# Kernel optimization log

Measured on AMD Instinct MI355X. Metric: run time of the kernel, lower is better.

The kernel has to match this reference:

```python
import jax, jax.numpy as jnp
import numpy as np

B, D, U = 64, 256, 256

def setup_inputs() -> dict:
    key = jax.random.key(0)
    ks = jax.random.split(key, 16)
    init_mu = 0.05
    inputs = jax.random.normal(ks[0], (B, D), jnp.float32)
    prev_state = 0.1 * jax.random.normal(ks[1], (B, U), jnp.float32)
    A = jax.random.normal(ks[2], (B, U, U), jnp.float32)
    # symmetric, diagonally boosted covariance-like state
    Sigma_state = 0.01 * (A + jnp.swapaxes(A, 1, 2)) + 0.1 * jnp.eye(U, dtype=jnp.float32)
    def w(k, shape):
        return init_mu * jax.random.normal(k, shape, jnp.float32)
    def s(k):
        return jax.random.uniform(k, (U,), jnp.float32, -4.5, -2.2)
    return {
        'inputs': inputs, 'prev_state': prev_state, 'Sigma_state': Sigma_state,
        'U_z': w(ks[3], (D, U)), 'uz_sigma': s(ks[4]), 'W_z': w(ks[5], (U, U)), 'wz_sigma': s(ks[6]),
        'U_r': w(ks[7], (D, U)), 'ur_sigma': s(ks[8]), 'W_r': w(ks[9], (U, U)), 'wr_sigma': s(ks[10]),
        'U_h': w(ks[11], (D, U)), 'uh_sigma': s(ks[12]), 'W_h': w(ks[13], (U, U)), 'wh_sigma': s(ks[14]),
    }

def _outer(a, b):  # [B,u],[B,u] -> [B,u,u]
    return a[:, :, None] * b[:, None, :]

def _quad(W, S):  # W^T @ S @ W, S is [B,u,u]
    return jnp.matmul(jnp.matmul(W.T, S), W)

def _x_sigma_w(x, sv):  # ||x||^2 * diag(softplus sigma)
    return jnp.sum(x * x, axis=1)[:, None, None] * jnp.diag(sv)

def _tr_sigma_w(S, sv):  # trace(S) * diag(softplus sigma)
    return jnp.trace(S, axis1=1, axis2=2)[:, None, None] * jnp.diag(sv)

def _hadamard_sigma(S1, S2, m1, m2):
    # S1*S2 + diag(m1) S2 diag(m1) + diag(m2) S1 diag(m2) as elementwise/broadcast
    return S1 * S2 + _outer(m1, m1) * S2 + _outer(m2, m2) * S1

def reference(inputs, prev_state, Sigma_state, U_z, uz_sigma, W_z, wz_sigma,
              U_r, ur_sigma, W_r, wr_sigma, U_h, uh_sigma, W_h, wh_sigma):
    sp = jax.nn.softplus
    # --- z gate ---
    az = inputs @ U_z + prev_state @ W_z
    z = jax.nn.sigmoid(az)
    gz = z * (1.0 - z)  # d sigmoid
    Sz = (_quad(W_z, Sigma_state) + _x_sigma_w(prev_state, sp(wz_sigma))
          + _tr_sigma_w(Sigma_state, sp(wz_sigma)) + _x_sigma_w(inputs, sp(uz_sigma)))
    Sigma_out_z = Sz * _outer(gz, gz)
    # --- r gate ---
    ar = inputs @ U_r + prev_state @ W_r
    r = jax.nn.sigmoid(ar)
    gr = r * (1.0 - r)
    Sr = (_quad(W_r, Sigma_state) + _x_sigma_w(prev_state, sp(wr_sigma))
          + _tr_sigma_w(Sigma_state, sp(wr_sigma)) + _x_sigma_w(inputs, sp(ur_sigma)))
    Sigma_out_r = Sr * _outer(gr, gr)
    # --- h candidate ---
    g_in = prev_state * r
    ah = inputs @ U_h + g_in @ W_h
    h = jnp.tanh(ah)
    gh = 1.0 - h * h  # d tanh
    sigma_g = _hadamard_sigma(Sigma_state, Sigma_out_r, prev_state, r)
    Sh = (_quad(W_h, sigma_g) + _x_sigma_w(g_in, sp(wh_sigma))
          + _tr_sigma_w(sigma_g, sp(wh_sigma)) + _x_sigma_w(inputs, sp(uh_sigma)))
    Sigma_out_h = Sh * _outer(gh, gh)
    # --- output combination ---
    mu_out = z * prev_state + (1.0 - z) * h
    sigma_a = _hadamard_sigma(Sigma_out_z, Sigma_state, z, prev_state)
    sigma_b = _hadamard_sigma(Sigma_out_z, Sigma_out_h, 1.0 - z, h)
    Sigma_out = (sigma_a + sigma_b
                 - Sigma_out_z * _outer(prev_state, h)
                 - Sigma_out_z * _outer(h, prev_state))
    Sigma_out = jnp.where(jnp.isnan(Sigma_out) | jnp.isinf(Sigma_out),
                          jnp.zeros_like(Sigma_out), Sigma_out)
    eye = jnp.eye(Sigma_out.shape[-1], dtype=Sigma_out.dtype)
    d = jnp.abs(jnp.diagonal(Sigma_out, axis1=1, axis2=2))
    Sigma_out = Sigma_out * (1.0 - eye) + d[:, :, None] * eye
    return mu_out, Sigma_out
```

## Files before the change

### kernel.cpp

```cpp
#include <hip/hip_runtime.h>
#include <math.h>

#define UDIM 256
#define BATCH 64
#define MATN 65536
#define PITCH 280

typedef __bf16 bf16x8 __attribute__((ext_vector_type(8)));
typedef float  f32x4  __attribute__((ext_vector_type(4)));

__device__ __forceinline__ float softplusf(float x) { return log1pf(expf(x)); }
__device__ __forceinline__ float sigmoidf_(float x) { return 1.f/(1.f+expf(-x)); }

__device__ __forceinline__ bf16x8 frag_load(const __bf16* base, int rt, int kt, int lane) {
  return *(const bf16x8*)(base + (((size_t)(rt*8 + kt))*64 + lane)*8);
}

__device__ __forceinline__ bf16x8 cvt8(const float* p) {
  const float4 f0 = *(const float4*)p;
  const float4 f1 = *(const float4*)(p + 4);
  bf16x8 v;
  v[0]=(__bf16)f0.x; v[1]=(__bf16)f0.y; v[2]=(__bf16)f0.z; v[3]=(__bf16)f0.w;
  v[4]=(__bf16)f1.x; v[5]=(__bf16)f1.y; v[6]=(__bf16)f1.z; v[7]=(__bf16)f1.w;
  return v;
}

__global__ __launch_bounds__(256) void prep_w(
    const float* __restrict__ Uz, const float* __restrict__ Wz,
    const float* __restrict__ Ur, const float* __restrict__ Wr,
    const float* __restrict__ Uh, const float* __restrict__ Wh,
    __bf16* __restrict__ Fu_z, __bf16* __restrict__ Fw_z,
    __bf16* __restrict__ Fu_r, __bf16* __restrict__ Fw_r,
    __bf16* __restrict__ Fu_h, __bf16* __restrict__ Fw_h,
    const float* __restrict__ S, const float* __restrict__ x,
    const float* __restrict__ prev, float* __restrict__ scal,
    __bf16* __restrict__ Sf)
{
  const int u = blockIdx.x;
  const int t = threadIdx.x;
  if (u >= 112) {
    const int c = u - 112;
    const int bx = c & 3, by = (c >> 2) & 3, b = c >> 4;
    const size_t sb = (size_t)b * MATN;
#pragma unroll
    for (int ss = 0; ss < 2; ++ss) {
      const int s = t + ss*256;
      const int chunk = s >> 6, lane = s & 63;
      const int rt_l = chunk >> 1, kt_l = chunk & 1;
      const int row = by*64 + rt_l*16 + (lane & 15);
      const int col = bx*64 + kt_l*32 + (lane >> 4)*8;
      const bf16x8 v = cvt8(S + sb + (size_t)row*UDIM + col);
      *(bf16x8*)(Sf + sb + (((size_t)((by*4 + rt_l)*8 + bx*2 + kt_l))*64 + lane)*8) = v;
    }
    return;
  }
  if (u >= 96) {
    const int blk = u - 96;
    const int b = blk*4 + (t >> 6), l = t & 63;
    const float4 xv = *(const float4*)(x + b*UDIM + l*4);
    float s0 = xv.x*xv.x + xv.y*xv.y + xv.z*xv.z + xv.w*xv.w;
    const float4 pv = *(const float4*)(prev + b*UDIM + l*4);
    float s1 = pv.x*pv.x + pv.y*pv.y + pv.z*pv.z + pv.w*pv.w;
    float s2 = 0.f;
#pragma unroll
    for (int e = 0; e < 4; ++e)
      s2 += S[(size_t)b*MATN + (size_t)(l*4 + e)*257];
    for (int off = 32; off; off >>= 1) {
      s0 += __shfl_down(s0, off);
      s1 += __shfl_down(s1, off);
      s2 += __shfl_down(s2, off);
    }
    if (l == 0) {
      atomicAdd(&scal[b], s0);
      atomicAdd(&scal[64 + b], s1);
      atomicAdd(&scal[128 + b], s2);
    }
    return;
  }
  const int mat = u >> 4, tl = u & 15;
  const int n0 = (tl & 3)*64, k0 = (tl >> 2)*64;
  const float* W; __bf16* F;
  switch (mat) {
    case 0: W = Uz; F = Fu_z; break;  case 1: W = Wz; F = Fw_z; break;
    case 2: W = Ur; F = Fu_r; break;  case 3: W = Wr; F = Fw_r; break;
    case 4: W = Uh; F = Fu_h; break;  default: W = Wh; F = Fw_h; break;
  }
  __shared__ float tile[64][65];
  const int tx = t & 15, ty = t >> 4;
#pragma unroll
  for (int rr = 0; rr < 4; ++rr) {
    const int row = ty*4 + rr;
    const float4 f = *(const float4*)(W + (size_t)(k0 + row)*UDIM + n0 + tx*4);
    tile[row][tx*4+0] = f.x; tile[row][tx*4+1] = f.y;
    tile[row][tx*4+2] = f.z; tile[row][tx*4+3] = f.w;
  }
  __syncthreads();
#pragma unroll
  for (int ss = 0; ss < 2; ++ss) {
    const int s = t + ss*256;
    const int rt_l = s >> 7, kt_l = (s >> 6) & 1, lane = s & 63;
    const int nl = rt_l*16 + (lane & 15), kb = kt_l*32 + (lane >> 4)*8;
    __align__(16) __bf16 tmp[8];
#pragma unroll
    for (int e = 0; e < 8; ++e) tmp[e] = (__bf16)tile[kb + e][nl];
    *(uint4*)(F + (((size_t)((((n0 >> 4) + rt_l)*8) + (k0 >> 5) + kt_l))*64 + lane)*8)
        = *(const uint4*)tmp;
  }
}

__global__ __launch_bounds__(256) void gates_zr(
    const float* __restrict__ x, const float* __restrict__ prev,
    const __bf16* __restrict__ Fu_z, const __bf16* __restrict__ Fw_z,
    const __bf16* __restrict__ Fu_r, const __bf16* __restrict__ Fw_r,
    float* __restrict__ zb, float* __restrict__ rb,
    float* __restrict__ gzb, float* __restrict__ grb,
    float* __restrict__ gin, float* __restrict__ scal)
{
  const int bid = blockIdx.x;
  const int gate = bid >> 4, jt = (bid >> 2) & 3, ni = bid & 3;
  const int t = threadIdx.x, w = t >> 6, l = t & 63, r = l & 15, q = l >> 4;
  const __bf16* FU = gate ? Fu_r : Fu_z;
  const __bf16* FW = gate ? Fw_r : Fw_z;
  const int mrow = w*16 + r;
  f32x4 acc = {};
#pragma unroll
  for (int ks = 0; ks < 16; ++ks) {
    const int k0 = ks*32;
    const float* asrc; const __bf16* B; int kk;
    if (k0 < 256) { asrc = x    + (size_t)mrow*UDIM + k0         + q*8; B = FU; kk = k0; }
    else          { asrc = prev + (size_t)mrow*UDIM + (k0 - 256) + q*8; B = FW; kk = k0 - 256; }
    const bf16x8 af = cvt8(asrc);
    const bf16x8 bv = frag_load(B, jt*4 + ni, kk >> 5, l);
    acc = __builtin_amdgcn_mfma_f32_16x16x32_bf16(af, bv, acc, 0, 0, 0);
  }
  const int n = jt*64 + ni*16 + r;
  if (gate == 0) {
#pragma unroll
    for (int v = 0; v < 4; ++v) {
      const int m = w*16 + q*4 + v;
      const float zv = sigmoidf_(acc[v]);
      zb[m*UDIM + n]  = zv;
      gzb[m*UDIM + n] = zv * (1.f - zv);
    }
  } else {
    float ggp[4];
#pragma unroll
    for (int v = 0; v < 4; ++v) {
      const int m = w*16 + q*4 + v;
      const float rv = sigmoidf_(acc[v]);
      const float pv = prev[m*UDIM + n];
      const float g2 = pv * rv;
      rb[m*UDIM + n]  = rv;
      grb[m*UDIM + n] = rv * (1.f - rv);
      gin[m*UDIM + n] = g2;
      ggp[v] = g2 * g2;
    }
#pragma unroll
    for (int s = 1; s < 16; s <<= 1)
#pragma unroll
      for (int v = 0; v < 4; ++v) ggp[v] += __shfl_xor(ggp[v], s);
    if (r == 0)
#pragma unroll
      for (int v = 0; v < 4; ++v)
        atomicAdd(&scal[192 + w*16 + q*4 + v], ggp[v]);
  }
}

__global__ __launch_bounds__(256, 2) void quad_zr_gh(
    const float* __restrict__ S, const __bf16* __restrict__ Sf,
    const float* __restrict__ prev,
    const float* __restrict__ rb, const float* __restrict__ gzb,
    const float* __restrict__ grb,
    const float* __restrict__ wz_s, const float* __restrict__ uz_s,
    const float* __restrict__ wr_s, const float* __restrict__ ur_s,
    const __bf16* __restrict__ Fw_z, const __bf16* __restrict__ Fw_r,
    float* __restrict__ scal, __bf16* __restrict__ Szb, __bf16* __restrict__ G,
    const float* __restrict__ x, const float* __restrict__ gin,
    const float* __restrict__ zb,
    const __bf16* __restrict__ Fu_h, const __bf16* __restrict__ Fw_h,
    float* __restrict__ hb, float* __restrict__ ghb, float* __restrict__ mu_out)
{
  const int bid = blockIdx.x;
  const int t = threadIdx.x, w = t >> 6, l = t & 63, r = l & 15, q = l >> 4;

  if (bid < 4) {
    const int jt = bid;
    const int mrow = w*16 + r;
    f32x4 acc[4] = {};
#pragma unroll
    for (int ks = 0; ks < 16; ++ks) {
      const int k0 = ks*32;
      const float* asrc; const __bf16* B; int kk;
      if (k0 < 256) { asrc = x   + (size_t)mrow*UDIM + k0         + q*8; B = Fu_h; kk = k0; }
      else          { asrc = gin + (size_t)mrow*UDIM + (k0 - 256) + q*8; B = Fw_h; kk = k0 - 256; }
      const bf16x8 af = cvt8(asrc);
#pragma unroll
      for (int ni = 0; ni < 4; ++ni) {
        const bf16x8 bv = frag_load(B, jt*4 + ni, kk >> 5, l);
        acc[ni] = __builtin_amdgcn_mfma_f32_16x16x32_bf16(af, bv, acc[ni], 0, 0, 0);
      }
    }
#pragma unroll
    for (int ni = 0; ni < 4; ++ni) {
      const int n = jt*64 + ni*16 + r;
#pragma unroll
      for (int v = 0; v < 4; ++v) {
        const int m = w*16 + q*4 + v;
        const float hv = tanhf(acc[ni][v]);
        const float zv = zb[m*UDIM + n];
        hb[m*UDIM + n]  = hv;
        ghb[m*UDIM + n] = 1.f - hv*hv;
        mu_out[m*UDIM + n] = zv * prev[m*UDIM + n] + (1.f - zv) * hv;
      }
    }
    return;
  }

  const int id = bid - 4;
  const int gater = (id < 256);
  const int rem = id & 255;
  const int sg = rem >> 6, b = rem & 63;
  const size_t sb = (size_t)b * MATN;
  const __bf16* Sfb = Sf + sb;
  const __bf16* FW = gater ? Fw_r : Fw_z;

  __shared__ __align__(16) __bf16 T[4*16*PITCH];

  f32x4 a[4][4] = {};
#pragma unroll
  for (int kt = 0; kt < 8; ++kt) {
    bf16x8 af[4];
#pragma unroll
    for (int sl = 0; sl < 4; ++sl) af[sl] = frag_load(FW, sg*4 + sl, kt, l);
#pragma unroll
    for (int ct = 0; ct < 4; ++ct) {
      const bf16x8 bv = frag_load(Sfb, w*4 + ct, kt, l);
#pragma unroll
      for (int sl = 0; sl < 4; ++sl)
        a[sl][ct] = __builtin_amdgcn_mfma_f32_16x16x32_bf16(af[sl], bv, a[sl][ct], 0, 0, 0);
    }
  }
#pragma unroll
  for (int sl = 0; sl < 4; ++sl)
#pragma unroll
    for (int ct = 0; ct < 4; ++ct)
#pragma unroll
      for (int v = 0; v < 4; ++v)
        T[sl*16*PITCH + (q*4 + v)*PITCH + w*64 + ct*16 + r] = (__bf16)a[sl][ct][v];
  __syncthreads();

  f32x4 qx[4][4] = {};
#pragma unroll
  for (int kt = 0; kt < 8; ++kt) {
    bf16x8 bw[4];
#pragma unroll
    for (int ct = 0; ct < 4; ++ct) bw[ct] = frag_load(FW, w*4 + ct, kt, l);
#pragma unroll
    for (int sl = 0; sl < 4; ++sl) {
      const bf16x8 at = *(const bf16x8*)&T[sl*16*PITCH + r*PITCH + kt*32 + q*8];
#pragma unroll
      for (int ct = 0; ct < 4; ++ct)
        qx[sl][ct] = __builtin_amdgcn_mfma_f32_16x16x32_bf16(at, bw[ct], qx[sl][ct], 0, 0, 0);
    }
  }

  const float xx = scal[b];
  const float dscal = scal[64 + b] + scal[128 + b];

  if (!gater) {
#pragma unroll
    for (int sl = 0; sl < 4; ++sl) {
      const int s4 = sg*4 + sl;
      const int ib = s4*16 + q*4;
      const f32x4 g4 = *(const f32x4*)(gzb + b*UDIM + ib);
      __align__(16) __bf16 o16[16];
#pragma unroll
      for (int ct = 0; ct < 4; ++ct) {
        const int j = (w*4 + ct)*16 + r;
        const float gj = gzb[b*UDIM + j];
#pragma unroll
        for (int v = 0; v < 4; ++v) {
          const int i = ib + v;
          float qv = qx[sl][ct][v];
          if (i == j) qv += dscal*softplusf(wz_s[i]) + xx*softplusf(uz_s[i]);
          o16[ct*4 + v] = (__bf16)(qv * g4[v] * gj);
        }
      }
      __bf16* dst = Szb + ((size_t)(b*16 + s4)*256 + t)*16;
      *(uint4*)dst       = *(const uint4*)&o16[0];
      *(uint4*)(dst + 8) = *(const uint4*)&o16[8];
    }
  } else {
    __syncthreads();
    float trg = 0.f;
#pragma unroll
    for (int sl = 0; sl < 4; ++sl) {
      const int s4 = sg*4 + sl;
      const int ib = s4*16 + q*4;
      const f32x4 g4 = *(const f32x4*)(grb + b*UDIM + ib);
      const f32x4 p4 = *(const f32x4*)(prev + b*UDIM + ib);
      const f32x4 r4 = *(const f32x4*)(rb + b*UDIM + ib);
#pragma unroll
      for (int ct = 0; ct < 4; ++ct) {
        const int j = (w*4 + ct)*16 + r;
        const float gj = grb[b*UDIM + j];
        const float pj = prev[b*UDIM + j];
        const float rj = rb[b*UDIM + j];
#pragma unroll
        for (int v = 0; v < 4; ++v) {
          const int i = ib + v;
          float qv = qx[sl][ct][v];
          if (i == j) qv += dscal*softplusf(wr_s[i]) + xx*softplusf(ur_s[i]);
          const float Sg = qv * g4[v] * gj;
          const float sv = S[sb + (size_t)i*UDIM + j];
          const float go = Sg*(sv + p4[v]*pj) + r4[v]*rj*sv;
          T[sl*16*PITCH + (q*4 + v)*PITCH + w*64 + ct*16 + r] = (__bf16)go;
          if (i == j) trg += go;
        }
      }
    }
    if (trg != 0.f) atomicAdd(&scal[256 + b], trg);
    __syncthreads();
#pragma unroll
    for (int sl = 0; sl < 4; ++sl)
#pragma unroll
      for (int ee = 0; ee < 2; ++ee) {
        const int e = t + ee*256;
        const int kt = e >> 6, le = e & 63;
        const uint4 vv = *(const uint4*)&T[sl*16*PITCH + (le & 15)*PITCH + kt*32 + (le >> 4)*8];
        *(uint4*)(G + sb + (((size_t)((sg*4 + sl)*8 + kt))*64 + le)*8) = vv;
      }
  }
}

__global__ __launch_bounds__(256, 2) void quad_h(
    const float* __restrict__ S, const __bf16* __restrict__ Szb,
    const float* __restrict__ prev, const float* __restrict__ zb,
    const float* __restrict__ hb, const float* __restrict__ ghb,
    const float* __restrict__ wh_s, const float* __restrict__ uh_s,
    const __bf16* __restrict__ Fw_h, const __bf16* __restrict__ G,
    const float* __restrict__ scal, float* __restrict__ out_sig)
{
  const int bid = blockIdx.x;
  const int sg = bid >> 6, b = bid & 63;
  const size_t sb = (size_t)b * MATN;
  const int t = threadIdx.x, w = t >> 6, l = t & 63, r = l & 15, q = l >> 4;
  const __bf16* Gb = G + sb;

  __shared__ __align__(16) __bf16 Th[2*16*PITCH];

  f32x4 ah[2][4] = {};
#pragma unroll
  for (int kt = 0; kt < 8; ++kt) {
    bf16x8 af[2];
#pragma unroll
    for (int sl = 0; sl < 2; ++sl) af[sl] = frag_load(Fw_h, sg*2 + sl, kt, l);
#pragma unroll
    for (int ct = 0; ct < 4; ++ct) {
      const bf16x8 bv = frag_load(Gb, w*4 + ct, kt, l);
#pragma unroll
      for (int sl = 0; sl < 2; ++sl)
        ah[sl][ct] = __builtin_amdgcn_mfma_f32_16x16x32_bf16(af[sl], bv, ah[sl][ct], 0, 0, 0);
    }
  }
#pragma unroll
  for (int sl = 0; sl < 2; ++sl)
#pragma unroll
    for (int ct = 0; ct < 4; ++ct)
#pragma unroll
      for (int v = 0; v < 4; ++v)
        Th[sl*16*PITCH + (q*4 + v)*PITCH + w*64 + ct*16 + r] = (__bf16)ah[sl][ct][v];
  __syncthreads();

  f32x4 qh[2][4] = {};
#pragma unroll
  for (int kt = 0; kt < 8; ++kt) {
    bf16x8 bw[4];
#pragma unroll
    for (int ct = 0; ct < 4; ++ct) bw[ct] = frag_load(Fw_h, w*4 + ct, kt, l);
#pragma unroll
    for (int sl = 0; sl < 2; ++sl) {
      const bf16x8 at = *(const bf16x8*)&Th[sl*16*PITCH + r*PITCH + kt*32 + q*8];
#pragma unroll
      for (int ct = 0; ct < 4; ++ct)
        qh[sl][ct] = __builtin_amdgcn_mfma_f32_16x16x32_bf16(at, bw[ct], qh[sl][ct], 0, 0, 0);
    }
  }

  const float xx = scal[b];
  const float dscal = scal[192 + b] + scal[256 + b];

#pragma unroll
  for (int sl = 0; sl < 2; ++sl) {
    const int s4 = sg*2 + sl;
    const int ib = s4*16 + q*4;

    const __bf16* szp = Szb + ((size_t)(b*16 + s4)*256 + t)*16;
    __align__(16) __bf16 sz16[16];
    *(uint4*)&sz16[0] = *(const uint4*)szp;
    *(uint4*)&sz16[8] = *(const uint4*)(szp + 8);

    const f32x4 g4 = *(const f32x4*)(ghb + b*UDIM + ib);
    const f32x4 p4 = *(const f32x4*)(prev + b*UDIM + ib);
    const f32x4 z4 = *(const f32x4*)(zb + b*UDIM + ib);
    const f32x4 h4 = *(const f32x4*)(hb + b*UDIM + ib);

#pragma unroll
    for (int ct = 0; ct < 4; ++ct) {
      const int j = (w*4 + ct)*16 + r;
      const float gj = ghb[b*UDIM + j];
      const float pj = prev[b*UDIM + j];
      const float zj = zb[b*UDIM + j];
      const float hj = hb[b*UDIM + j];
#pragma unroll
      for (int v = 0; v < 4; ++v) {
        const int i = ib + v;
        float qv = qh[sl][ct][v];
        if (i == j) qv += dscal*softplusf(wh_s[i]) + xx*softplusf(uh_s[i]);
        const float Sg = qv * g4[v] * gj;
        const float sv = S[sb + (size_t)i*UDIM + j];
        const float sz = (float)sz16[ct*4 + v];
        float val = sv*(sz + z4[v]*zj)
                  + sz*(p4[v] - h4[v])*(pj - hj)
                  + Sg*(sz + (1.f - z4[v])*(1.f - zj));
        if (!isfinite(val)) val = 0.f;
        if (i == j) val = fabsf(val);
        out_sig[sb + (size_t)i*UDIM + j] = val;
      }
    }
  }
}

extern "C" void kernel_launch(void* const* d_in, const int* in_sizes, int n_in,
                              void* d_out, int out_size, void* d_ws, size_t ws_size,
                              hipStream_t stream) {
  const float* x    = (const float*)d_in[0];
  const float* prev = (const float*)d_in[1];
  const float* S    = (const float*)d_in[2];
  const float* Uz   = (const float*)d_in[3];
  const float* uz_s = (const float*)d_in[4];
  const float* Wz   = (const float*)d_in[5];
  const float* wz_s = (const float*)d_in[6];
  const float* Ur   = (const float*)d_in[7];
  const float* ur_s = (const float*)d_in[8];
  const float* Wr   = (const float*)d_in[9];
  const float* wr_s = (const float*)d_in[10];
  const float* Uh   = (const float*)d_in[11];
  const float* uh_s = (const float*)d_in[12];
  const float* Wh   = (const float*)d_in[13];
  const float* wh_s = (const float*)d_in[14];

  float* out_mu  = (float*)d_out;
  float* out_sig = out_mu + BATCH*UDIM;

  float* ws   = (float*)d_ws;
  float* zb   = ws;
  float* rb   = zb  + BATCH*UDIM;
  float* gzb  = rb  + BATCH*UDIM;
  float* grb  = gzb + BATCH*UDIM;
  float* gin  = grb + BATCH*UDIM;
  float* hb   = gin + BATCH*UDIM;
  float* ghb  = hb  + BATCH*UDIM;
  float* scal = ghb + BATCH*UDIM;
  __bf16* bws  = (__bf16*)(scal + 512);
  __bf16* Fu_z = bws;
  __bf16* Fw_z = Fu_z + MATN;
  __bf16* Fu_r = Fw_z + MATN;
  __bf16* Fw_r = Fu_r + MATN;
  __bf16* Fu_h = Fw_r + MATN;
  __bf16* Fw_h = Fu_h + MATN;
  const size_t BIG = (size_t)BATCH * MATN;
  __bf16* Szb = Fw_h + MATN;
  __bf16* G   = Szb + BIG;
  __bf16* Sf  = G + BIG;

  hipMemsetAsync(scal, 0, 512*sizeof(float), stream);

  prep_w<<<dim3(1136), 256, 0, stream>>>(Uz, Wz, Ur, Wr, Uh, Wh,
      Fu_z, Fw_z, Fu_r, Fw_r, Fu_h, Fw_h, S, x, prev, scal, Sf);
  gates_zr<<<dim3(32), 256, 0, stream>>>(x, prev,
      Fu_z, Fw_z, Fu_r, Fw_r, zb, rb, gzb, grb, gin, scal);
  quad_zr_gh<<<dim3(516), 256, 0, stream>>>(S, Sf, prev, rb, gzb, grb,
      wz_s, uz_s, wr_s, ur_s, Fw_z, Fw_r, scal, Szb, G,
      x, gin, zb, Fu_h, Fw_h, hb, ghb, out_mu);
  quad_h<<<dim3(512), 256, 0, stream>>>(S, Szb, prev, zb, hb, ghb,
      wh_s, uh_s, Fw_h, G, scal, out_sig);
}
```

Measured before the change: 172.0 us.

## Fuse four kernels into one persistent kernel with software grid barriers

Replaces the prep, gate, quad_zr and quad_h launches with a single 512-block kernel that separates the phases with a hierarchical atomic grid barrier. It also swaps the atomicAdd reductions for per-slot partial writes that are summed later, so the scalar buffer no longer needs a memset. The aim is to remove launch gaps and the tail idle time between dependent stages. In exchange, all 512 blocks must be co-resident (two per CU) or the barrier will deadlock, and spin-waiting adds its own overhead.

```diff
diff --git a/kernel.cpp b/kernel.cpp
--- a/kernel.cpp
+++ b/kernel.cpp
@@ -5,6 +5,9 @@
 #define BATCH 64
 #define MATN 65536
 #define PITCH 280
+#define NBLK 512
+#define GG_BASE 256
+#define TRG_BASE 1280
 
 typedef __bf16 bf16x8 __attribute__((ext_vector_type(8)));
 typedef float  f32x4  __attribute__((ext_vector_type(4)));
@@ -25,407 +28,411 @@
   return v;
 }
 
-__global__ __launch_bounds__(256) void prep_w(
-    const float* __restrict__ Uz, const float* __restrict__ Wz,
-    const float* __restrict__ Ur, const float* __restrict__ Wr,
-    const float* __restrict__ Uh, const float* __restrict__ Wh,
+__device__ __forceinline__ void gridbar(unsigned int* cnt, int bid, int t) {
+  __syncthreads();
+  if (t == 0) {
+    __threadfence();
+    unsigned int* lc = cnt + (bid & 7);
+    unsigned int* gc = cnt + 15;
+    if (atomicAdd(lc, 1u) == (unsigned)(NBLK/8 - 1)) atomicAdd(gc, 1u);
+    while (__hip_atomic_load(gc, __ATOMIC_RELAXED, __HIP_MEMORY_SCOPE_AGENT) < 8u)
+      __builtin_amdgcn_s_sleep(2);
+    __threadfence();
+  }
+  __syncthreads();
+}
+
+__global__ __launch_bounds__(256, 2) void fused(
+    const float* __restrict__ x, const float* __restrict__ prev,
+    const float* __restrict__ S,
+    const float* __restrict__ Uz, const float* __restrict__ uz_s,
+    const float* __restrict__ Wz, const float* __restrict__ wz_s,
+    const float* __restrict__ Ur, const float* __restrict__ ur_s,
+    const float* __restrict__ Wr, const float* __restrict__ wr_s,
+    const float* __restrict__ Uh, const float* __restrict__ uh_s,
+    const float* __restrict__ Wh, const float* __restrict__ wh_s,
+    float* __restrict__ out_mu, float* __restrict__ out_sig,
+    float* __restrict__ zb, float* __restrict__ rb,
+    float* __restrict__ gzb, float* __restrict__ grb,
+    float* __restrict__ gin, float* __restrict__ hb, float* __restrict__ ghb,
+    float* __restrict__ scal, unsigned int* __restrict__ bar,
     __bf16* __restrict__ Fu_z, __bf16* __restrict__ Fw_z,
     __bf16* __restrict__ Fu_r, __bf16* __restrict__ Fw_r,
     __bf16* __restrict__ Fu_h, __bf16* __restrict__ Fw_h,
-    const float* __restrict__ S, const float* __restrict__ x,
-    const float* __restrict__ prev, float* __restrict__ scal,
-    __bf16* __restrict__ Sf)
+    __bf16* __restrict__ Szb, __bf16* __restrict__ G, __bf16* __restrict__ Sf)
 {
-  const int u = blockIdx.x;
+  const int bid = blockIdx.x;
   const int t = threadIdx.x;
-  if (u >= 112) {
-    const int c = u - 112;
-    const int bx = c & 3, by = (c >> 2) & 3, b = c >> 4;
-    const size_t sb = (size_t)b * MATN;
+  const int w = t >> 6, l = t & 63, r = l & 15, q = l >> 4;
+
+  __shared__ __align__(16) unsigned char LDSU[4*16*PITCH*2];
+
+  if (bid < 96) {
+    const int mat = bid >> 4, tl = bid & 15;
+    const int n0 = (tl & 3)*64, k0 = (tl >> 2)*64;
+    const float* W; __bf16* F;
+    switch (mat) {
+      case 0: W = Uz; F = Fu_z; break;  case 1: W = Wz; F = Fw_z; break;
+      case 2: W = Ur; F = Fu_r; break;  case 3: W = Wr; F = Fw_r; break;
+      case 4: W = Uh; F = Fu_h; break;  default: W = Wh; F = Fw_h; break;
+    }
+    float (*tile)[65] = (float (*)[65])LDSU;
+    const int tx = t & 15, ty = t >> 4;
+#pragma unroll
+    for (int rr = 0; rr < 4; ++rr) {
+      const int row = ty*4 + rr;
+      const float4 f = *(const float4*)(W + (size_t)(k0 + row)*UDIM + n0 + tx*4);
+      tile[row][tx*4+0] = f.x; tile[row][tx*4+1] = f.y;
+      tile[row][tx*4+2] = f.z; tile[row][tx*4+3] = f.w;
+    }
+    __syncthreads();
 #pragma unroll
     for (int ss = 0; ss < 2; ++ss) {
       const int s = t + ss*256;
-      const int chunk = s >> 6, lane = s & 63;
-      const int rt_l = chunk >> 1, kt_l = chunk & 1;
-      const int row = by*64 + rt_l*16 + (lane & 15);
-      const int col = bx*64 + kt_l*32 + (lane >> 4)*8;
-      const bf16x8 v = cvt8(S + sb + (size_t)row*UDIM + col);
-      *(bf16x8*)(Sf + sb + (((size_t)((by*4 + rt_l)*8 + bx*2 + kt_l))*64 + lane)*8) = v;
-    }
-    return;
-  }
-  if (u >= 96) {
-    const int blk = u - 96;
-    const int b = blk*4 + (t >> 6), l = t & 63;
-    const float4 xv = *(const float4*)(x + b*UDIM + l*4);
+      const int rt_l = s >> 7, kt_l = (s >> 6) & 1, lane = s & 63;
+      const int nl = rt_l*16 + (lane & 15), kb = kt_l*32 + (lane >> 4)*8;
+      __align__(16) __bf16 tmp[8];
+#pragma unroll
+      for (int e = 0; e < 8; ++e) tmp[e] = (__bf16)tile[kb + e][nl];
+      *(uint4*)(F + (((size_t)((((n0 >> 4) + rt_l)*8) + (k0 >> 5) + kt_l))*64 + lane)*8)
+          = *(const uint4*)tmp;
+    }
+    __syncthreads();
+  } else if (bid < 112) {
+    const int blk = bid - 96;
+    const int b0 = blk*4 + (t >> 6);
+    const float4 xv = *(const float4*)(x + b0*UDIM + l*4);
     float s0 = xv.x*xv.x + xv.y*xv.y + xv.z*xv.z + xv.w*xv.w;
-    const float4 pv = *(const float4*)(prev + b*UDIM + l*4);
+    const float4 pv = *(const float4*)(prev + b0*UDIM + l*4);
     float s1 = pv.x*pv.x + pv.y*pv.y + pv.z*pv.z + pv.w*pv.w;
     float s2 = 0.f;
 #pragma unroll
     for (int e = 0; e < 4; ++e)
-      s2 += S[(size_t)b*MATN + (size_t)(l*4 + e)*257];
+      s2 += S[(size_t)b0*MATN + (size_t)(l*4 + e)*257];
     for (int off = 32; off; off >>= 1) {
       s0 += __shfl_down(s0, off);
       s1 += __shfl_down(s1, off);
       s2 += __shfl_down(s2, off);
     }
-    if (l == 0) {
-      atomicAdd(&scal[b], s0);
-      atomicAdd(&scal[64 + b], s1);
-      atomicAdd(&scal[128 + b], s2);
-    }
-    return;
-  }
-  const int mat = u >> 4, tl = u & 15;
-  const int n0 = (tl & 3)*64, k0 = (tl >> 2)*64;
-  const float* W; __bf16* F;
-  switch (mat) {
-    case 0: W = Uz; F = Fu_z; break;  case 1: W = Wz; F = Fw_z; break;
-    case 2: W = Ur; F = Fu_r; break;  case 3: W = Wr; F = Fw_r; break;
-    case 4: W = Uh; F = Fu_h; break;  default: W = Wh; F = Fw_h; break;
-  }
-  __shared__ float tile[64][65];
-  const int tx = t & 15, ty = t >> 4;
-#pragma unroll
-  for (int rr = 0; rr < 4; ++rr) {
-    const int row = ty*4 + rr;
-    const float4 f = *(const float4*)(W + (size_t)(k0 + row)*UDIM + n0 + tx*4);
-    tile[row][tx*4+0] = f.x; tile[row][tx*4+1] = f.y;
-    tile[row][tx*4+2] = f.z; tile[row][tx*4+3] = f.w;
-  }
-  __syncthreads();
-#pragma unroll
-  for (int ss = 0; ss < 2; ++ss) {
-    const int s = t + ss*256;
-    const int rt_l = s >> 7, kt_l = (s >> 6) & 1, lane = s & 63;
-    const int nl = rt_l*16 + (lane & 15), kb = kt_l*32 + (lane >> 4)*8;
-    __align__(16) __bf16 tmp[8];
-#pragma unroll
-    for (int e = 0; e < 8; ++e) tmp[e] = (__bf16)tile[kb + e][nl];
-    *(uint4*)(F + (((size_t)((((n0 >> 4) + rt_l)*8) + (k0 >> 5) + kt_l))*64 + lane)*8)
-        = *(const uint4*)tmp;
-  }
-}
-
-__global__ __launch_bounds__(256) void gates_zr(
-    const float* __restrict__ x, const float* __restrict__ prev,
-    const __bf16* __restrict__ Fu_z, const __bf16* __restrict__ Fw_z,
-    const __bf16* __restrict__ Fu_r, const __bf16* __restrict__ Fw_r,
-    float* __restrict__ zb, float* __restrict__ rb,
-    float* __restrict__ gzb, float* __restrict__ grb,
-    float* __restrict__ gin, float* __restrict__ scal)
-{
-  const int bid = blockIdx.x;
-  const int gate = bid >> 4, jt = (bid >> 2) & 3, ni = bid & 3;
-  const int t = threadIdx.x, w = t >> 6, l = t & 63, r = l & 15, q = l >> 4;
-  const __bf16* FU = gate ? Fu_r : Fu_z;
+    if (l == 0) { scal[b0] = s0; scal[64 + b0] = s1; scal[128 + b0] = s2; }
+  }
+  {
+    const int bb = bid & 63, hi = bid >> 6;
+    const size_t csb = (size_t)bb * MATN;
+#pragma unroll
+    for (int e2 = 0; e2 < 2; ++e2) {
+      const int c = (bb << 4) | (hi << 1) | e2;
+      const int bx = c & 3, by = (c >> 2) & 3;
+#pragma unroll
+      for (int ss = 0; ss < 2; ++ss) {
+        const int s = t + ss*256;
+        const int chunk = s >> 6, lane = s & 63;
+        const int rt_l = chunk >> 1, kt_l = chunk & 1;
+        const int row = by*64 + rt_l*16 + (lane & 15);
+        const int col = bx*64 + kt_l*32 + (lane >> 4)*8;
+        const bf16x8 v = cvt8(S + csb + (size_t)row*UDIM + col);
+        *(bf16x8*)(Sf + csb + (((size_t)((by*4 + rt_l)*8 + bx*2 + kt_l))*64 + lane)*8) = v;
+      }
+    }
+  }
+  gridbar(bar, bid, t);
+
+  const int gate = bid >> 8;
+  const int rem8 = bid & 255;
+  const int sg = rem8 >> 6, b = rem8 & 63;
+  const size_t sb = (size_t)b * MATN;
   const __bf16* FW = gate ? Fw_r : Fw_z;
-  const int mrow = w*16 + r;
-  f32x4 acc = {};
-#pragma unroll
-  for (int ks = 0; ks < 16; ++ks) {
-    const int k0 = ks*32;
-    const float* asrc; const __bf16* B; int kk;
-    if (k0 < 256) { asrc = x    + (size_t)mrow*UDIM + k0         + q*8; B = FU; kk = k0; }
-    else          { asrc = prev + (size_t)mrow*UDIM + (k0 - 256) + q*8; B = FW; kk = k0 - 256; }
-    const bf16x8 af = cvt8(asrc);
-    const bf16x8 bv = frag_load(B, jt*4 + ni, kk >> 5, l);
-    acc = __builtin_amdgcn_mfma_f32_16x16x32_bf16(af, bv, acc, 0, 0, 0);
-  }
-  const int n = jt*64 + ni*16 + r;
-  if (gate == 0) {
-#pragma unroll
-    for (int v = 0; v < 4; ++v) {
-      const int m = w*16 + q*4 + v;
-      const float zv = sigmoidf_(acc[v]);
-      zb[m*UDIM + n]  = zv;
-      gzb[m*UDIM + n] = zv * (1.f - zv);
-    }
-  } else {
-    float ggp[4];
-#pragma unroll
-    for (int v = 0; v < 4; ++v) {
-      const int m = w*16 + q*4 + v;
-      const float rv = sigmoidf_(acc[v]);
-      const float pv = prev[m*UDIM + n];
-      const float g2 = pv * rv;
-      rb[m*UDIM + n]  = rv;
-      grb[m*UDIM + n] = rv * (1.f - rv);
-      gin[m*UDIM + n] = g2;
-      ggp[v] = g2 * g2;
-    }
-#pragma unroll
-    for (int s = 1; s < 16; s <<= 1)
-#pragma unroll
-      for (int v = 0; v < 4; ++v) ggp[v] += __shfl_xor(ggp[v], s);
-    if (r == 0)
-#pragma unroll
-      for (int v = 0; v < 4; ++v)
-        atomicAdd(&scal[192 + w*16 + q*4 + v], ggp[v]);
-  }
-}
-
-__global__ __launch_bounds__(256, 2) void quad_zr_gh(
-    const float* __restrict__ S, const __bf16* __restrict__ Sf,
-    const float* __restrict__ prev,
-    const float* __restrict__ rb, const float* __restrict__ gzb,
-    const float* __restrict__ grb,
-    const float* __restrict__ wz_s, const float* __restrict__ uz_s,
-    const float* __restrict__ wr_s, const float* __restrict__ ur_s,
-    const __bf16* __restrict__ Fw_z, const __bf16* __restrict__ Fw_r,
-    float* __restrict__ scal, __bf16* __restrict__ Szb, __bf16* __restrict__ G,
-    const float* __restrict__ x, const float* __restrict__ gin,
-    const float* __restrict__ zb,
-    const __bf16* __restrict__ Fu_h, const __bf16* __restrict__ Fw_h,
-    float* __restrict__ hb, float* __restrict__ ghb, float* __restrict__ mu_out)
-{
-  const int bid = blockIdx.x;
-  const int t = threadIdx.x, w = t >> 6, l = t & 63, r = l & 15, q = l >> 4;
-
-  if (bid < 4) {
-    const int jt = bid;
+  __bf16* T = (__bf16*)LDSU;
+
+  if (bid < 32) {
+    const int gg_ = bid >> 4, jt_ = (bid >> 2) & 3, ni_ = bid & 3;
+    const __bf16* FU_ = gg_ ? Fu_r : Fu_z;
+    const __bf16* FW_ = gg_ ? Fw_r : Fw_z;
     const int mrow = w*16 + r;
-    f32x4 acc[4] = {};
+    f32x4 acc = {};
 #pragma unroll
     for (int ks = 0; ks < 16; ++ks) {
       const int k0 = ks*32;
-      const float* asrc; const __bf16* B; int kk;
-      if (k0 < 256) { asrc = x   + (size_t)mrow*UDIM + k0         + q*8; B = Fu_h; kk = k0; }
-      else          { asrc = gin + (size_t)mrow*UDIM + (k0 - 256) + q*8; B = Fw_h; kk = k0 - 256; }
+      const float* asrc; const __bf16* Bm; int kk;
+      if (k0 < 256) { asrc = x    + (size_t)mrow*UDIM + k0         + q*8; Bm = FU_; kk = k0; }
+      else          { asrc = prev + (size_t)mrow*UDIM + (k0 - 256) + q*8; Bm = FW_; kk = k0 - 256; }
       const bf16x8 af = cvt8(asrc);
-#pragma unroll
-      for (int ni = 0; ni < 4; ++ni) {
-        const bf16x8 bv = frag_load(B, jt*4 + ni, kk >> 5, l);
-        acc[ni] = __builtin_amdgcn_mfma_f32_16x16x32_bf16(af, bv, acc[ni], 0, 0, 0);
-      }
-    }
-#pragma unroll
-    for (int ni = 0; ni < 4; ++ni) {
-      const int n = jt*64 + ni*16 + r;
+      const bf16x8 bv = frag_load(Bm, jt_*4 + ni_, kk >> 5, l);
+      acc = __builtin_amdgcn_mfma_f32_16x16x32_bf16(af, bv, acc, 0, 0, 0);
+    }
+    const int n = jt_*64 + ni_*16 + r;
+    if (gg_ == 0) {
 #pragma unroll
       for (int v = 0; v < 4; ++v) {
         const int m = w*16 + q*4 + v;
-        const float hv = tanhf(acc[ni][v]);
+        const float zv = sigmoidf_(acc[v]);
+        zb[m*UDIM + n]  = zv;
+        gzb[m*UDIM + n] = zv * (1.f - zv);
+      }
+    } else {
+      float ggp[4];
+#pragma unroll
+      for (int v = 0; v < 4; ++v) {
+        const int m = w*16 + q*4 + v;
+        const float rv = sigmoidf_(acc[v]);
+        const float pv = prev[m*UDIM + n];
+        const float g2 = pv * rv;
+        rb[m*UDIM + n]  = rv;
+        grb[m*UDIM + n] = rv * (1.f - rv);
+        gin[m*UDIM + n] = g2;
+        ggp[v] = g2 * g2;
+      }
+#pragma unroll
+      for (int s2 = 1; s2 < 16; s2 <<= 1)
+#pragma unroll
+        for (int v = 0; v < 4; ++v) ggp[v] += __shfl_xor(ggp[v], s2);
+      if (r == 0)
+#pragma unroll
+        for (int v = 0; v < 4; ++v)
+          scal[GG_BASE + (w*16 + q*4 + v)*16 + (jt_*4 + ni_)] = ggp[v];
+    }
+  }
+
+  {
+    const __bf16* Sfb = Sf + sb;
+    f32x4 a[4][4] = {};
+#pragma unroll
+    for (int kt = 0; kt < 8; ++kt) {
+      bf16x8 af4[4];
+#pragma unroll
+      for (int sl = 0; sl < 4; ++sl) af4[sl] = frag_load(FW, sg*4 + sl, kt, l);
+#pragma unroll
+      for (int ct = 0; ct < 4; ++ct) {
+        const bf16x8 bv = frag_load(Sfb, w*4 + ct, kt, l);
+#pragma unroll
+        for (int sl = 0; sl < 4; ++sl)
+          a[sl][ct] = __builtin_amdgcn_mfma_f32_16x16x32_bf16(af4[sl], bv, a[sl][ct], 0, 0, 0);
+      }
+    }
+#pragma unroll
+    for (int sl = 0; sl < 4; ++sl)
+#pragma unroll
+      for (int ct = 0; ct < 4; ++ct)
+#pragma unroll
+        for (int v = 0; v < 4; ++v)
+          T[sl*16*PITCH + (q*4 + v)*PITCH + w*64 + ct*16 + r] = (__bf16)a[sl][ct][v];
+  }
+  gridbar(bar + 16, bid, t);
+
+  if (bid >= 32 && bid < 36) {
+    const int jt_h = bid - 32;
+    const int mrow = w*16 + r;
+    f32x4 acch[4] = {};
+#pragma unroll
+    for (int ks = 0; ks < 16; ++ks) {
+      const int k0 = ks*32;
+      const float* asrc; const __bf16* Bm; int kk;
+      if (k0 < 256) { asrc = x   + (size_t)mrow*UDIM + k0         + q*8; Bm = Fu_h; kk = k0; }
+      else          { asrc = gin + (size_t)mrow*UDIM + (k0 - 256) + q*8; Bm = Fw_h; kk = k0 - 256; }
+      const bf16x8 af = cvt8(asrc);
+#pragma unroll
+      for (int ni = 0; ni < 4; ++ni) {
+        const bf16x8 bv = frag_load(Bm, jt_h*4 + ni, kk >> 5, l);
+        acch[ni] = __builtin_amdgcn_mfma_f32_16x16x32_bf16(af, bv, acch[ni], 0, 0, 0);
+      }
+    }
+#pragma unroll
+    for (int ni = 0; ni < 4; ++ni) {
+      const int n = jt_h*64 + ni*16 + r;
+#pragma unroll
+      for (int v = 0; v < 4; ++v) {
+        const int m = w*16 + q*4 + v;
+        const float hv = tanhf(acch[ni][v]);
         const float zv = zb[m*UDIM + n];
         hb[m*UDIM + n]  = hv;
         ghb[m*UDIM + n] = 1.f - hv*hv;
-        mu_out[m*UDIM + n] = zv * prev[m*UDIM + n] + (1.f - zv) * hv;
-      }
-    }
-    return;
-  }
-
-  const int id = bid - 4;
-  const int gater = (id < 256);
-  const int rem = id & 255;
-  const int sg = rem >> 6, b = rem & 63;
-  const size_t sb = (size_t)b * MATN;
-  const __bf16* Sfb = Sf + sb;
-  const __bf16* FW = gater ? Fw_r : Fw_z;
-
-  __shared__ __align__(16) __bf16 T[4*16*PITCH];
-
-  f32x4 a[4][4] = {};
-#pragma unroll
-  for (int kt = 0; kt < 8; ++kt) {
-    bf16x8 af[4];
-#pragma unroll
-    for (int sl = 0; sl < 4; ++sl) af[sl] = frag_load(FW, sg*4 + sl, kt, l);
-#pragma unroll
-    for (int ct = 0; ct < 4; ++ct) {
-      const bf16x8 bv = frag_load(Sfb, w*4 + ct, kt, l);
+        out_mu[m*UDIM + n] = zv * prev[m*UDIM + n] + (1.f - zv) * hv;
+      }
+    }
+  }
+
+  {
+    f32x4 qx[4][4] = {};
+#pragma unroll
+    for (int kt = 0; kt < 8; ++kt) {
+      bf16x8 bw[4];
+#pragma unroll
+      for (int ct = 0; ct < 4; ++ct) bw[ct] = frag_load(FW, w*4 + ct, kt, l);
+#pragma unroll
+      for (int sl = 0; sl < 4; ++sl) {
+        const bf16x8 at = *(const bf16x8*)&T[sl*16*PITCH + r*PITCH + kt*32 + q*8];
+#pragma unroll
+        for (int ct = 0; ct < 4; ++ct)
+          qx[sl][ct] = __builtin_amdgcn_mfma_f32_16x16x32_bf16(at, bw[ct], qx[sl][ct], 0, 0, 0);
+      }
+    }
+
+    const float xx = scal[b];
+    const float dsc = scal[64 + b] + scal[128 + b];
+
+    if (gate == 0) {
+#pragma unroll
+      for (int sl = 0; sl < 4; ++sl) {
+        const int s4 = sg*4 + sl;
+        const int ib = s4*16 + q*4;
+        const f32x4 g4 = *(const f32x4*)(gzb + b*UDIM + ib);
+        __align__(16) __bf16 o16[16];
+#pragma unroll
+        for (int ct = 0; ct < 4; ++ct) {
+          const int j = (w*4 + ct)*16 + r;
+          const float gj = gzb[b*UDIM + j];
+#pragma unroll
+          for (int v = 0; v < 4; ++v) {
+            const int i = ib + v;
+            float qv = qx[sl][ct][v];
+            if (i == j) qv += dsc*softplusf(wz_s[i]) + xx*softplusf(uz_s[i]);
+            o16[ct*4 + v] = (__bf16)(qv * g4[v] * gj);
+          }
+        }
+        __bf16* dst = Szb + ((size_t)(b*16 + s4)*256 + t)*16;
+        *(uint4*)dst       = *(const uint4*)&o16[0];
+        *(uint4*)(dst + 8) = *(const uint4*)&o16[8];
+      }
+    } else {
+      __syncthreads();
+      float trgs[4] = {0.f, 0.f, 0.f, 0.f};
+#pragma unroll
+      for (int sl = 0; sl < 4; ++sl) {
+        const int s4 = sg*4 + sl;
+        const int ib = s4*16 + q*4;
+        const f32x4 g4 = *(const f32x4*)(grb + b*UDIM + ib);
+        const f32x4 p4 = *(const f32x4*)(prev + b*UDIM + ib);
+        const f32x4 r4 = *(const f32x4*)(rb + b*UDIM + ib);
+#pragma unroll
+        for (int ct = 0; ct < 4; ++ct) {
+          const int j = (w*4 + ct)*16 + r;
+          const float gj = grb[b*UDIM + j];
+          const float pj = prev[b*UDIM + j];
+          const float rj = rb[b*UDIM + j];
+#pragma unroll
+          for (int v = 0; v < 4; ++v) {
+            const int i = ib + v;
+            float qv = qx[sl][ct][v];
+            if (i == j) qv += dsc*softplusf(wr_s[i]) + xx*softplusf(ur_s[i]);
+            const float Sg = qv * g4[v] * gj;
+            const float sv = S[sb + (size_t)i*UDIM + j];
+            const float go = Sg*(sv + p4[v]*pj) + r4[v]*rj*sv;
+            T[sl*16*PITCH + (q*4 + v)*PITCH + w*64 + ct*16 + r] = (__bf16)go;
+            if (i == j) trgs[sl] += go;
+          }
+        }
+      }
+      if (w == sg) {
+#pragma unroll
+        for (int sl = 0; sl < 4; ++sl)
+#pragma unroll
+          for (int s2 = 1; s2 < 64; s2 <<= 1) trgs[sl] += __shfl_xor(trgs[sl], s2);
+        if (l == 0)
+#pragma unroll
+          for (int sl = 0; sl < 4; ++sl)
+            scal[TRG_BASE + b*16 + sg*4 + sl] = trgs[sl];
+      }
+      __syncthreads();
 #pragma unroll
       for (int sl = 0; sl < 4; ++sl)
-        a[sl][ct] = __builtin_amdgcn_mfma_f32_16x16x32_bf16(af[sl], bv, a[sl][ct], 0, 0, 0);
-    }
-  }
-#pragma unroll
-  for (int sl = 0; sl < 4; ++sl)
-#pragma unroll
-    for (int ct = 0; ct < 4; ++ct)
-#pragma unroll
-      for (int v = 0; v < 4; ++v)
-        T[sl*16*PITCH + (q*4 + v)*PITCH + w*64 + ct*16 + r] = (__bf16)a[sl][ct][v];
-  __syncthreads();
-
-  f32x4 qx[4][4] = {};
-#pragma unroll
-  for (int kt = 0; kt < 8; ++kt) {
-    bf16x8 bw[4];
-#pragma unroll
-    for (int ct = 0; ct < 4; ++ct) bw[ct] = frag_load(FW, w*4 + ct, kt, l);
-#pragma unroll
-    for (int sl = 0; sl < 4; ++sl) {
-      const bf16x8 at = *(const bf16x8*)&T[sl*16*PITCH + r*PITCH + kt*32 + q*8];
+#pragma unroll
+        for (int ee = 0; ee < 2; ++ee) {
+          const int e = t + ee*256;
+          const int kt = e >> 6, le = e & 63;
+          const uint4 vv = *(const uint4*)&T[sl*16*PITCH + (le & 15)*PITCH + kt*32 + (le >> 4)*8];
+          *(uint4*)(G + sb + (((size_t)((sg*4 + sl)*8 + kt))*64 + le)*8) = vv;
+        }
+    }
+  }
+  gridbar(bar + 32, bid, t);
+
+  {
+    const int b3 = bid & 63, sg2 = bid >> 6;
+    const size_t sb3 = (size_t)b3 * MATN;
+    const __bf16* Gb = G + sb3;
+    __bf16* Th = (__bf16*)LDSU;
+
+    f32x4 ah[2][4] = {};
+#pragma unroll
+    for (int kt = 0; kt < 8; ++kt) {
+      bf16x8 af2[2];
+#pragma unroll
+      for (int sl = 0; sl < 2; ++sl) af2[sl] = frag_load(Fw_h, sg2*2 + sl, kt, l);
+#pragma unroll
+      for (int ct = 0; ct < 4; ++ct) {
+        const bf16x8 bv = frag_load(Gb, w*4 + ct, kt, l);
+#pragma unroll
+        for (int sl = 0; sl < 2; ++sl)
+          ah[sl][ct] = __builtin_amdgcn_mfma_f32_16x16x32_bf16(af2[sl], bv, ah[sl][ct], 0, 0, 0);
+      }
+    }
+#pragma unroll
+    for (int sl = 0; sl < 2; ++sl)
 #pragma unroll
       for (int ct = 0; ct < 4; ++ct)
-        qx[sl][ct] = __builtin_amdgcn_mfma_f32_16x16x32_bf16(at, bw[ct], qx[sl][ct], 0, 0, 0);
-    }
-  }
-
-  const float xx = scal[b];
-  const float dscal = scal[64 + b] + scal[128 + b];
-
-  if (!gater) {
-#pragma unroll
-    for (int sl = 0; sl < 4; ++sl) {
-      const int s4 = sg*4 + sl;
+#pragma unroll
+        for (int v = 0; v < 4; ++v)
+          Th[sl*16*PITCH + (q*4 + v)*PITCH + w*64 + ct*16 + r] = (__bf16)ah[sl][ct][v];
+    __syncthreads();
+
+    f32x4 qh[2][4] = {};
+#pragma unroll
+    for (int kt = 0; kt < 8; ++kt) {
+      bf16x8 bw2[4];
+#pragma unroll
+      for (int ct = 0; ct < 4; ++ct) bw2[ct] = frag_load(Fw_h, w*4 + ct, kt, l);
+#pragma unroll
+      for (int sl = 0; sl < 2; ++sl) {
+        const bf16x8 at = *(const bf16x8*)&Th[sl*16*PITCH + r*PITCH + kt*32 + q*8];
+#pragma unroll
+        for (int ct = 0; ct < 4; ++ct)
+          qh[sl][ct] = __builtin_amdgcn_mfma_f32_16x16x32_bf16(at, bw2[ct], qh[sl][ct], 0, 0, 0);
+      }
+    }
+
+    const float xx3 = scal[b3];
+    float ggs = 0.f, trs = 0.f;
+#pragma unroll
+    for (int u2 = 0; u2 < 16; ++u2) {
+      ggs += scal[GG_BASE + b3*16 + u2];
+      trs += scal[TRG_BASE + b3*16 + u2];
+    }
+    const float dsc3 = ggs + trs;
+
+#pragma unroll
+    for (int sl = 0; sl < 2; ++sl) {
+      const int s4 = sg2*2 + sl;
       const int ib = s4*16 + q*4;
-      const f32x4 g4 = *(const f32x4*)(gzb + b*UDIM + ib);
-      __align__(16) __bf16 o16[16];
+      const __bf16* szp = Szb + ((size_t)(b3*16 + s4)*256 + t)*16;
+      __align__(16) __bf16 sz16[16];
+      *(uint4*)&sz16[0] = *(const uint4*)szp;
+      *(uint4*)&sz16[8] = *(const uint4*)(szp + 8);
+      const f32x4 g4 = *(const f32x4*)(ghb + b3*UDIM + ib);
+      const f32x4 p4 = *(const f32x4*)(prev + b3*UDIM + ib);
+      const f32x4 z4 = *(const f32x4*)(zb + b3*UDIM + ib);
+      const f32x4 h4 = *(const f32x4*)(hb + b3*UDIM + ib);
 #pragma unroll
       for (int ct = 0; ct < 4; ++ct) {
         const int j = (w*4 + ct)*16 + r;
-        const float gj = gzb[b*UDIM + j];
+        const float gj = ghb[b3*UDIM + j];
+        const float pj = prev[b3*UDIM + j];
+        const float zj = zb[b3*UDIM + j];
+        const float hj = hb[b3*UDIM + j];
 #pragma unroll
         for (int v = 0; v < 4; ++v) {
           const int i = ib + v;
-          float qv = qx[sl][ct][v];
-          if (i == j) qv += dscal*softplusf(wz_s[i]) + xx*softplusf(uz_s[i]);
-          o16[ct*4 + v] = (__bf16)(qv * g4[v] * gj);
+          float qv = qh[sl][ct][v];
+          if (i == j) qv += dsc3*softplusf(wh_s[i]) + xx3*softplusf(uh_s[i]);
+          const float Sg = qv * g4[v] * gj;
+          const float sv = S[sb3 + (size_t)i*UDIM + j];
+          const float sz = (float)sz16[ct*4 + v];
+          float val = sv*(sz + z4[v]*zj)
+                    + sz*(p4[v] - h4[v])*(pj - hj)
+                    + Sg*(sz + (1.f - z4[v])*(1.f - zj));
+          if (!isfinite(val)) val = 0.f;
+          if (i == j) val = fabsf(val);
+          out_sig[sb3 + (size_t)i*UDIM + j] = val;
         }
-      }
-      __bf16* dst = Szb + ((size_t)(b*16 + s4)*256 + t)*16;
-      *(uint4*)dst       = *(const uint4*)&o16[0];
-      *(uint4*)(dst + 8) = *(const uint4*)&o16[8];
-    }
-  } else {
-    __syncthreads();
-    float trg = 0.f;
-#pragma unroll
-    for (int sl = 0; sl < 4; ++sl) {
-      const int s4 = sg*4 + sl;
-      const int ib = s4*16 + q*4;
-      const f32x4 g4 = *(const f32x4*)(grb + b*UDIM + ib);
-      const f32x4 p4 = *(const f32x4*)(prev + b*UDIM + ib);
-      const f32x4 r4 = *(const f32x4*)(rb + b*UDIM + ib);
-#pragma unroll
-      for (int ct = 0; ct < 4; ++ct) {
-        const int j = (w*4 + ct)*16 + r;
-        const float gj = grb[b*UDIM + j];
-        const float pj = prev[b*UDIM + j];
-        const float rj = rb[b*UDIM + j];
-#pragma unroll
-        for (int v = 0; v < 4; ++v) {
-          const int i = ib + v;
-          float qv = qx[sl][ct][v];
-          if (i == j) qv += dscal*softplusf(wr_s[i]) + xx*softplusf(ur_s[i]);
-          const float Sg = qv * g4[v] * gj;
-          const float sv = S[sb + (size_t)i*UDIM + j];
-          const float go = Sg*(sv + p4[v]*pj) + r4[v]*rj*sv;
-          T[sl*16*PITCH + (q*4 + v)*PITCH + w*64 + ct*16 + r] = (__bf16)go;
-          if (i == j) trg += go;
-        }
-      }
-    }
-    if (trg != 0.f) atomicAdd(&scal[256 + b], trg);
-    __syncthreads();
-#pragma unroll
-    for (int sl = 0; sl < 4; ++sl)
-#pragma unroll
-      for (int ee = 0; ee < 2; ++ee) {
-        const int e = t + ee*256;
-        const int kt = e >> 6, le = e & 63;
-        const uint4 vv = *(const uint4*)&T[sl*16*PITCH + (le & 15)*PITCH + kt*32 + (le >> 4)*8];
-        *(uint4*)(G + sb + (((size_t)((sg*4 + sl)*8 + kt))*64 + le)*8) = vv;
-      }
-  }
-}
-
-__global__ __launch_bounds__(256, 2) void quad_h(
-    const float* __restrict__ S, const __bf16* __restrict__ Szb,
-    const float* __restrict__ prev, const float* __restrict__ zb,
-    const float* __restrict__ hb, const float* __restrict__ ghb,
-    const float* __restrict__ wh_s, const float* __restrict__ uh_s,
-    const __bf16* __restrict__ Fw_h, const __bf16* __restrict__ G,
-    const float* __restrict__ scal, float* __restrict__ out_sig)
-{
-  const int bid = blockIdx.x;
-  const int sg = bid >> 6, b = bid & 63;
-  const size_t sb = (size_t)b * MATN;
-  const int t = threadIdx.x, w = t >> 6, l = t & 63, r = l & 15, q = l >> 4;
-  const __bf16* Gb = G + sb;
-
-  __shared__ __align__(16) __bf16 Th[2*16*PITCH];
-
-  f32x4 ah[2][4] = {};
-#pragma unroll
-  for (int kt = 0; kt < 8; ++kt) {
-    bf16x8 af[2];
-#pragma unroll
-    for (int sl = 0; sl < 2; ++sl) af[sl] = frag_load(Fw_h, sg*2 + sl, kt, l);
-#pragma unroll
-    for (int ct = 0; ct < 4; ++ct) {
-      const bf16x8 bv = frag_load(Gb, w*4 + ct, kt, l);
-#pragma unroll
-      for (int sl = 0; sl < 2; ++sl)
-        ah[sl][ct] = __builtin_amdgcn_mfma_f32_16x16x32_bf16(af[sl], bv, ah[sl][ct], 0, 0, 0);
-    }
-  }
-#pragma unroll
-  for (int sl = 0; sl < 2; ++sl)
-#pragma unroll
-    for (int ct = 0; ct < 4; ++ct)
-#pragma unroll
-      for (int v = 0; v < 4; ++v)
-        Th[sl*16*PITCH + (q*4 + v)*PITCH + w*64 + ct*16 + r] = (__bf16)ah[sl][ct][v];
-  __syncthreads();
-
-  f32x4 qh[2][4] = {};
-#pragma unroll
-  for (int kt = 0; kt < 8; ++kt) {
-    bf16x8 bw[4];
-#pragma unroll
-    for (int ct = 0; ct < 4; ++ct) bw[ct] = frag_load(Fw_h, w*4 + ct, kt, l);
-#pragma unroll
-    for (int sl = 0; sl < 2; ++sl) {
-      const bf16x8 at = *(const bf16x8*)&Th[sl*16*PITCH + r*PITCH + kt*32 + q*8];
-#pragma unroll
-      for (int ct = 0; ct < 4; ++ct)
-        qh[sl][ct] = __builtin_amdgcn_mfma_f32_16x16x32_bf16(at, bw[ct], qh[sl][ct], 0, 0, 0);
-    }
-  }
-
-  const float xx = scal[b];
-  const float dscal = scal[192 + b] + scal[256 + b];
-
-#pragma unroll
-  for (int sl = 0; sl < 2; ++sl) {
-    const int s4 = sg*2 + sl;
-    const int ib = s4*16 + q*4;
-
-    const __bf16* szp = Szb + ((size_t)(b*16 + s4)*256 + t)*16;
-    __align__(16) __bf16 sz16[16];
-    *(uint4*)&sz16[0] = *(const uint4*)szp;
-    *(uint4*)&sz16[8] = *(const uint4*)(szp + 8);
-
-    const f32x4 g4 = *(const f32x4*)(ghb + b*UDIM + ib);
-    const f32x4 p4 = *(const f32x4*)(prev + b*UDIM + ib);
-    const f32x4 z4 = *(const f32x4*)(zb + b*UDIM + ib);
-    const f32x4 h4 = *(const f32x4*)(hb + b*UDIM + ib);
-
-#pragma unroll
-    for (int ct = 0; ct < 4; ++ct) {
-      const int j = (w*4 + ct)*16 + r;
-      const float gj = ghb[b*UDIM + j];
-      const float pj = prev[b*UDIM + j];
-      const float zj = zb[b*UDIM + j];
-      const float hj = hb[b*UDIM + j];
-#pragma unroll
-      for (int v = 0; v < 4; ++v) {
-        const int i = ib + v;
-        float qv = qh[sl][ct][v];
-        if (i == j) qv += dscal*softplusf(wh_s[i]) + xx*softplusf(uh_s[i]);
-        const float Sg = qv * g4[v] * gj;
-        const float sv = S[sb + (size_t)i*UDIM + j];
-        const float sz = (float)sz16[ct*4 + v];
-        float val = sv*(sz + z4[v]*zj)
-                  + sz*(p4[v] - h4[v])*(pj - hj)
-                  + Sg*(sz + (1.f - z4[v])*(1.f - zj));
-        if (!isfinite(val)) val = 0.f;
-        if (i == j) val = fabsf(val);
-        out_sig[sb + (size_t)i*UDIM + j] = val;
       }
     }
   }
@@ -462,7 +469,8 @@
   float* hb   = gin + BATCH*UDIM;
   float* ghb  = hb  + BATCH*UDIM;
   float* scal = ghb + BATCH*UDIM;
-  __bf16* bws  = (__bf16*)(scal + 512);
+  unsigned int* bar = (unsigned int*)(scal + 2304);
+  __bf16* bws  = (__bf16*)(scal + 2304 + 64);
   __bf16* Fu_z = bws;
   __bf16* Fw_z = Fu_z + MATN;
   __bf16* Fu_r = Fw_z + MATN;
@@ -474,15 +482,10 @@
   __bf16* G   = Szb + BIG;
   __bf16* Sf  = G + BIG;
 
-  hipMemsetAsync(scal, 0, 512*sizeof(float), stream);
-
-  prep_w<<<dim3(1136), 256, 0, stream>>>(Uz, Wz, Ur, Wr, Uh, Wh,
-      Fu_z, Fw_z, Fu_r, Fw_r, Fu_h, Fw_h, S, x, prev, scal, Sf);
-  gates_zr<<<dim3(32), 256, 0, stream>>>(x, prev,
-      Fu_z, Fw_z, Fu_r, Fw_r, zb, rb, gzb, grb, gin, scal);
-  quad_zr_gh<<<dim3(516), 256, 0, stream>>>(S, Sf, prev, rb, gzb, grb,
-      wz_s, uz_s, wr_s, ur_s, Fw_z, Fw_r, scal, Szb, G,
-      x, gin, zb, Fu_h, Fw_h, hb, ghb, out_mu);
-  quad_h<<<dim3(512), 256, 0, stream>>>(S, Szb, prev, zb, hb, ghb,
-      wh_s, uh_s, Fw_h, G, scal, out_sig);
+  (void)hipMemsetAsync(bar, 0, 64*sizeof(unsigned int), stream);
+
+  fused<<<dim3(NBLK), 256, 0, stream>>>(x, prev, S,
+      Uz, uz_s, Wz, wz_s, Ur, ur_s, Wr, wr_s, Uh, uh_s, Wh, wh_s,
+      out_mu, out_sig, zb, rb, gzb, grb, gin, hb, ghb, scal, bar,
+      Fu_z, Fw_z, Fu_r, Fw_r, Fu_h, Fw_h, Szb, G, Sf);
 }
```

Result: slower. 284.0 us (+65.1%).
